# Performance work log

Measured on AMD Instinct MI355X. Metric: run time of the kernel, lower is better.

The kernel has to match this reference:

```python
import jax, jax.numpy as jnp
import numpy as np

NUM_EMB = 1_000_000
DIM = 64
COMPRESSION = 0.25
HSIZE = int(NUM_EMB * DIM * COMPRESSION)  # 16_000_000
NUM_BAGS = 4096
BAG_LEN = 50
TOTAL = NUM_BAGS * BAG_LEN  # 204800


def setup_inputs() -> dict:
    key = jax.random.key(0)
    k_w, k_x = jax.random.split(key)
    # learned compressed weight vector (torch.nn.init.normal_)
    hashed_weight = jax.random.normal(k_w, (HSIZE,), dtype=jnp.float32)
    # linear_hash_func: idx[i, j] = (i * embedding_dim + j) % HSIZE, shape [NUM_EMB, DIM]
    weight_idx = (jnp.arange(NUM_EMB * DIM, dtype=jnp.int32) % HSIZE).reshape(NUM_EMB, DIM)
    # flat bag of indices + bag-start offsets (fixed-length bags of BAG_LEN)
    x = jax.random.randint(k_x, (TOTAL,), 0, NUM_EMB, dtype=jnp.int32)
    offsets = jnp.arange(NUM_BAGS, dtype=jnp.int32) * BAG_LEN
    return {"hashed_weight": hashed_weight, "weight_idx": weight_idx, "x": x, "offsets": offsets}


def reference(hashed_weight, weight_idx, x, offsets):
    # Fused double indirection: only gather the rows actually looked up,
    # never materializing the full [NUM_EMB, DIM] virtual table.
    rows = weight_idx[x]              # [T, D] int32 indices into hashed_weight
    emb = hashed_weight[rows]         # [T, D]
    T = x.shape[0]
    # segment id of each lookup = which bag it belongs to (embedding_bag semantics,
    # include_last_offset=False: last bag runs to the end)
    seg = jnp.searchsorted(offsets, jnp.arange(T, dtype=offsets.dtype), side="right") - 1
    return jax.ops.segment_sum(emb, seg, num_segments=offsets.shape[0])  # [NUM_BAGS, D]
```

## Files before the change

kernel.cpp:

```cpp
#include <hip/hip_runtime.h>


#define DIM 64
#define HSIZE 16000000

__global__ __launch_bounds__(256) void hash_embedding_bag_kernel(
    const float* __restrict__ hashed_weight,
    const int* __restrict__ x,
    const int* __restrict__ offsets,
    float* __restrict__ out,
    int num_bags, int total)
{
    const int wave = threadIdx.x >> 6;
    const int lane = threadIdx.x & 63;
    const int bag  = blockIdx.x * 4 + wave;
    if (bag >= num_bags) return;

    const int start = offsets[bag];
    const int end   = (bag + 1 < num_bags) ? offsets[bag + 1] : total;
    const int n     = end - start;

    float acc = 0.0f;
    int t = 0;
    for (; t + 5 <= n; t += 5) {
        int b0 = (x[start + t + 0] * DIM) % HSIZE;
        int b1 = (x[start + t + 1] * DIM) % HSIZE;
        int b2 = (x[start + t + 2] * DIM) % HSIZE;
        int b3 = (x[start + t + 3] * DIM) % HSIZE;
        int b4 = (x[start + t + 4] * DIM) % HSIZE;
        float v0 = hashed_weight[b0 + lane];
        float v1 = hashed_weight[b1 + lane];
        float v2 = hashed_weight[b2 + lane];
        float v3 = hashed_weight[b3 + lane];
        float v4 = hashed_weight[b4 + lane];
        acc += v0 + v1 + v2 + v3 + v4;
    }
    for (; t < n; ++t) {
        int b0 = (x[start + t] * DIM) % HSIZE;
        acc += hashed_weight[b0 + lane];
    }

    out[bag * DIM + lane] = acc;
}

extern "C" void kernel_launch(void* const* d_in, const int* in_sizes, int n_in,
                              void* d_out, int out_size, void* d_ws, size_t ws_size,
                              hipStream_t stream) {
    const float* hashed_weight = (const float*)d_in[0];
    const int* x       = (const int*)d_in[2];
    const int* offsets = (const int*)d_in[3];
    float* out = (float*)d_out;

    const int total    = in_sizes[2];
    const int num_bags = in_sizes[3];

    const int waves_per_block = 4;
    const int blocks = (num_bags + waves_per_block - 1) / waves_per_block;
    hash_embedding_bag_kernel<<<blocks, waves_per_block * 64, 0, stream>>>(
        hashed_weight, x, offsets, out, num_bags, total);
}
```

Baseline: 318.4 us.

## Gather rows with float4 loads, four rows per wave, and reduce with shuffles

```diff
diff --git a/kernel.cpp b/kernel.cpp
--- a/kernel.cpp
+++ b/kernel.cpp
@@ -16,31 +16,54 @@
     const int bag  = blockIdx.x * 4 + wave;
     if (bag >= num_bags) return;
 
+    const int g = lane >> 4;
+    const int s = lane & 15;
+
     const int start = offsets[bag];
     const int end   = (bag + 1 < num_bags) ? offsets[bag + 1] : total;
     const int n     = end - start;
 
-    float acc = 0.0f;
-    int t = 0;
-    for (; t + 5 <= n; t += 5) {
-        int b0 = (x[start + t + 0] * DIM) % HSIZE;
-        int b1 = (x[start + t + 1] * DIM) % HSIZE;
-        int b2 = (x[start + t + 2] * DIM) % HSIZE;
-        int b3 = (x[start + t + 3] * DIM) % HSIZE;
-        int b4 = (x[start + t + 4] * DIM) % HSIZE;
-        float v0 = hashed_weight[b0 + lane];
-        float v1 = hashed_weight[b1 + lane];
-        float v2 = hashed_weight[b2 + lane];
-        float v3 = hashed_weight[b3 + lane];
-        float v4 = hashed_weight[b4 + lane];
-        acc += v0 + v1 + v2 + v3 + v4;
-    }
-    for (; t < n; ++t) {
-        int b0 = (x[start + t] * DIM) % HSIZE;
-        acc += hashed_weight[b0 + lane];
+    float4 acc = make_float4(0.f, 0.f, 0.f, 0.f);
+    const float* __restrict__ hw = hashed_weight;
+
+    if (n == 50) {
+        #pragma unroll
+        for (int r = 0; r < 48; r += 4) {
+            int   xi   = x[start + r + g];
+            int   base = (xi * DIM) % HSIZE;
+            float4 v   = *reinterpret_cast<const float4*>(hw + base + s * 4);
+            acc.x += v.x; acc.y += v.y; acc.z += v.z; acc.w += v.w;
+        }
+        if (g < 2) {
+            int   xi   = x[start + 48 + g];
+            int   base = (xi * DIM) % HSIZE;
+            float4 v   = *reinterpret_cast<const float4*>(hw + base + s * 4);
+            acc.x += v.x; acc.y += v.y; acc.z += v.z; acc.w += v.w;
+        }
+    } else {
+        for (int r = 0; r < n; r += 4) {
+            int row = r + g;
+            if (row < n) {
+                int   xi   = x[start + row];
+                int   base = (xi * DIM) % HSIZE;
+                float4 v   = *reinterpret_cast<const float4*>(hw + base + s * 4);
+                acc.x += v.x; acc.y += v.y; acc.z += v.z; acc.w += v.w;
+            }
+        }
     }
 
-    out[bag * DIM + lane] = acc;
+    acc.x += __shfl_xor(acc.x, 16);
+    acc.y += __shfl_xor(acc.y, 16);
+    acc.z += __shfl_xor(acc.z, 16);
+    acc.w += __shfl_xor(acc.w, 16);
+    acc.x += __shfl_xor(acc.x, 32);
+    acc.y += __shfl_xor(acc.y, 32);
+    acc.z += __shfl_xor(acc.z, 32);
+    acc.w += __shfl_xor(acc.w, 32);
+
+    if (lane < 16) {
+        *reinterpret_cast<float4*>(out + bag * DIM + s * 4) = acc;
+    }
 }
 
 extern "C" void kernel_launch(void* const* d_in, const int* in_sizes, int n_in,
```

Result: no change. 318.5 us (+0.0%).
